# Kernel optimization log

Measured on AMD Instinct MI355X. Metric: run time of the kernel, lower is better.

Reference implementation:

```python
import jax, jax.numpy as jnp
import numpy as np

B, H, W = 8, 256, 256
NF = 64          # num_feat
E = 12           # num_expert
D = NF * 4       # token dim = 256
CD = D * E       # expanded dim = 3072


def _lrelu(x):
    return jnp.where(x >= 0, x, 0.2 * x)


def _conv(x, w, stride, pad):
    return jax.lax.conv_general_dilated(
        x, w, (stride, stride), [(pad, pad), (pad, pad)],
        dimension_numbers=('NCHW', 'OIHW', 'NCHW'))


def _bn(x, g, b):
    # training-mode BatchNorm2d: batch statistics over (N, H, W)
    m = jnp.mean(x, axis=(0, 2, 3), keepdims=True)
    v = jnp.var(x, axis=(0, 2, 3), keepdims=True)
    xn = (x - m) * jax.lax.rsqrt(v + 1e-5)
    return xn * g[None, :, None, None] + b[None, :, None, None]


def setup_inputs() -> dict:
    key = jax.random.key(0)
    ks = jax.random.split(key, 16)
    s = 0.05
    d = {}
    d['x'] = jax.random.normal(ks[0], (B, 3, H, W), jnp.float32)
    d['conv0_w'] = jax.random.normal(ks[1], (NF, 3, 3, 3)) * s
    d['conv0_b'] = jnp.zeros((NF,))
    d['conv1_w'] = jax.random.normal(ks[2], (NF, NF, 4, 4)) * s
    d['bn1_g'] = jnp.ones((NF,)); d['bn1_b'] = jnp.zeros((NF,))
    d['conv2_w'] = jax.random.normal(ks[3], (2 * NF, NF, 3, 3)) * s
    d['bn2_g'] = jnp.ones((2 * NF,)); d['bn2_b'] = jnp.zeros((2 * NF,))
    d['conv3_w'] = jax.random.normal(ks[4], (2 * NF, 2 * NF, 4, 4)) * s
    d['bn3_g'] = jnp.ones((2 * NF,)); d['bn3_b'] = jnp.zeros((2 * NF,))
    d['conv4_w'] = jax.random.normal(ks[5], (4 * NF, 2 * NF, 3, 3)) * s
    d['bn4_g'] = jnp.ones((4 * NF,)); d['bn4_b'] = jnp.zeros((4 * NF,))
    d['conv5_w'] = jax.random.normal(ks[6], (4 * NF, 4 * NF, 3, 3)) * s
    d['bn5_g'] = jnp.ones((4 * NF,)); d['bn5_b'] = jnp.zeros((4 * NF,))
    d['conv6_w'] = jax.random.normal(ks[7], (4 * NF, 4 * NF, 3, 3)) * s
    d['bn6_g'] = jnp.ones((4 * NF,)); d['bn6_b'] = jnp.zeros((4 * NF,))
    d['w_gating'] = jax.random.normal(ks[8], (D, E))          # torch.randn init
    d['body_w'] = jax.random.normal(ks[9], (D, CD)) * s       # Linear(c_dim, c_dim*blocks)
    d['body_b'] = jnp.zeros((CD,))
    d['ortho_w'] = jax.random.normal(ks[10], (1, 1, CD))      # OrthorTransform weight
    d['cls_w1'] = jax.random.normal(ks[11], (D, NF // 2)) * s # shared classifier
    d['cls_b1'] = jnp.zeros((NF // 2,))
    d['cls_w2'] = jax.random.normal(ks[12], (NF // 2, 1)) * s
    d['cls_b2'] = jnp.zeros((1,))
    return d


def reference(x, conv0_w, conv0_b, conv1_w, bn1_g, bn1_b, conv2_w, bn2_g, bn2_b,
              conv3_w, bn3_g, bn3_b, conv4_w, bn4_g, bn4_b, conv5_w, bn5_g, bn5_b,
              conv6_w, bn6_g, bn6_b, w_gating, body_w, body_b, ortho_w,
              cls_w1, cls_b1, cls_w2, cls_b2):
    # --- FE conv stack ---
    h = _lrelu(_conv(x, conv0_w, 1, 1) + conv0_b[None, :, None, None])
    h = _lrelu(_bn(_conv(h, conv1_w, 2, 1), bn1_g, bn1_b))
    h = _lrelu(_bn(_conv(h, conv2_w, 1, 1), bn2_g, bn2_b))
    h = _lrelu(_bn(_conv(h, conv3_w, 2, 1), bn3_g, bn3_b))
    h = _lrelu(_bn(_conv(h, conv4_w, 1, 1), bn4_g, bn4_b))
    h = _lrelu(_bn(_conv(h, conv5_w, 1, 1), bn5_g, bn5_b))
    h = _lrelu(_bn(_conv(h, conv6_w, 1, 1), bn6_g, bn6_b))
    b, c, hh, ww = h.shape
    tok = h.reshape(b, c, hh * ww).transpose(0, 2, 1)            # (B, N, D)
    # --- softmax router ---
    routing = jax.nn.softmax(jnp.einsum('bnd,de->bne', tok, w_gating), axis=-1)
    # --- CodeReduction: Linear + lrelu, OrthorTransform multiply, lrelu ---
    feat = _lrelu(tok @ body_w + body_b)                         # (B, N, E*D)
    feat = _lrelu(feat * ortho_w)
    feat = feat.reshape(b, hh * ww, E, D)                        # torch.split chunks
    # --- shared expert MLP on every chunk (all classifiers alias one module) ---
    hid = _lrelu(jnp.einsum('bned,df->bnef', feat, cls_w1) + cls_b1)
    outs = (jnp.einsum('bnef,fo->bneo', hid, cls_w2) + cls_b2)[..., 0]  # (B,N,E)
    # --- top-1 select (equivalent to the torch.where cascade) ---
    idx = jnp.argmax(routing, axis=-1, keepdims=True)
    output = jnp.take_along_axis(outs, idx, axis=-1)             # (B, N, 1)
    return output
```

## Files before the change

kernel.cpp:

```cpp
#include <hip/hip_runtime.h>

__device__ __forceinline__ float lrelu(float x) { return x >= 0.f ? x : 0.2f * x; }

typedef const __attribute__((address_space(1))) void* gas_ptr;
typedef __attribute__((address_space(3))) void* las_ptr;

__global__ __launch_bounds__(256) void conv0_k(const float* __restrict__ x,
                                               const float* __restrict__ w,
                                               const float* __restrict__ bias,
                                               float* __restrict__ out) {
    __shared__ float sIn[3][34][34];
    __shared__ float sW[27][16];
    const int H = 256;
    int tid = threadIdx.x, tx = tid & 31, ty = tid >> 5;
    int tX = (blockIdx.x & 7) * 32, tY = (blockIdx.x >> 3) * 32;
    int b = blockIdx.y, cog = blockIdx.z * 16;
    float acc[4][16] = {};
    const float* inB = x + (size_t)b * 3 * H * H;
    for (int idx = tid; idx < 3 * 1156; idx += 256) {
        int ci = idx / 1156, r = idx % 1156, iy = r / 34, ix = r % 34;
        int gy = tY - 1 + iy, gx = tX - 1 + ix;
        float v = 0.f;
        if ((unsigned)gy < 256u && (unsigned)gx < 256u)
            v = inB[(ci * H + gy) * H + gx];
        sIn[ci][iy][ix] = v;
    }
    for (int idx = tid; idx < 27 * 16; idx += 256) {
        int co = idx & 15, rest = idx >> 4;
        sW[rest][co] = w[(cog + co) * 27 + rest];
    }
    __syncthreads();
#pragma unroll
    for (int ci = 0; ci < 3; ci++)
#pragma unroll
        for (int dy = 0; dy < 3; dy++)
#pragma unroll
            for (int dx = 0; dx < 3; dx++) {
                float a0 = sIn[ci][ty + dy][tx + dx];
                float a1 = sIn[ci][ty + 8 + dy][tx + dx];
                float a2 = sIn[ci][ty + 16 + dy][tx + dx];
                float a3 = sIn[ci][ty + 24 + dy][tx + dx];
                const float* wp = sW[ci * 9 + dy * 3 + dx];
#pragma unroll
                for (int co = 0; co < 16; co++) {
                    float wv = wp[co];
                    acc[0][co] += a0 * wv; acc[1][co] += a1 * wv;
                    acc[2][co] += a2 * wv; acc[3][co] += a3 * wv;
                }
            }
    float* outB = out + (size_t)(b * 64 + cog) * 67080;
#pragma unroll
    for (int co = 0; co < 16; co++) {
        float bv = bias[cog + co];
#pragma unroll
        for (int r = 0; r < 4; r++)
            outB[(size_t)co * 67080 + (size_t)(tY + ty + 8 * r + 1) * 260 +
                 tX + tx + 1] = lrelu(acc[r][co] + bv);
    }
}

template <int COG, int RPT>
__device__ __forceinline__ void stats_epi(float (&acc)[RPT][COG], float2* sRed,
                                          double2* part, int cog, int slotBase,
                                          int S, int tid) {
    const int lane = tid & 63, wv = tid >> 6;
    float s[COG], q[COG];
#pragma unroll
    for (int c = 0; c < COG; c++) {
        float ss = 0.f, qq = 0.f;
#pragma unroll
        for (int j = 0; j < RPT; j++) { float v = acc[j][c]; ss += v; qq += v * v; }
        s[c] = ss; q[c] = qq;
    }
#pragma unroll
    for (int off = 32; off; off >>= 1)
#pragma unroll
        for (int c = 0; c < COG; c++) {
            s[c] += __shfl_xor(s[c], off);
            q[c] += __shfl_xor(q[c], off);
        }
    if (lane == 0)
#pragma unroll
        for (int c = 0; c < COG; c++) sRed[wv * COG + c] = make_float2(s[c], q[c]);
    __syncthreads();
    if (tid < COG) {
        double ss = 0.0, qq = 0.0;
#pragma unroll
        for (int wvi = 0; wvi < 4; wvi++) {
            float2 p = sRed[wvi * COG + tid];
            ss += (double)p.x; qq += (double)p.y;
        }
        int slot = slotBase + blockIdx.y * gridDim.x + blockIdx.x;
        part[(size_t)(cog + tid) * S + slot] = make_double2(ss, qq);
    }
}

template <int COG>
__global__ __launch_bounds__(256) void c4x4p_k(const float* __restrict__ in,
                                               const float* __restrict__ w,
                                               float* __restrict__ out,
                                               double2* __restrict__ part,
                                               int slotBase, int S,
                                               int Cin, int Cout, int Hin,
                                               int Hp, int Wp,
                                               int oHp, int oWp, int oOff) {
    __shared__ float sIn[2][4488];
    __shared__ float sW[2][16 * COG];
    __shared__ float2 sRed[4 * COG];
    const int Hout = Hin >> 1;
    const int tid = threadIdx.x, tx = tid & 31, ty = tid >> 5;
    const int tpr = Hout >> 5;
    const int tX = (blockIdx.x % tpr) * 32, tY = (blockIdx.x / tpr) * 32;
    const int b = blockIdx.y, cog = blockIdx.z * COG;
    const int HWin = Hp * Wp;
    const float* inB = in + (size_t)b * Cin * HWin;
    const int wvbase = tid & ~63;

    int gOff[5]; int lOff[5]; bool act[5];
#pragma unroll
    for (int r = 0; r < 5; r++) {
        int idx = tid + r * 256;
        bool a = idx < 1122;
        int row = idx / 17, c4 = idx % 17;
        gOff[r] = a ? ((2 * tY + row) * Wp + 2 * tX + 4 * c4) : 0;
        lOff[r] = (r * 256 + wvbase) * 4;
        act[r] = a;
    }
    const int wco = tid % COG, wt = tid / COG;
    const int wgo = ((cog + wco) * Cin) * 16 + wt;
    const bool wact = tid < 16 * COG;

    float acc[4][COG];
#pragma unroll
    for (int j = 0; j < 4; j++)
#pragma unroll
        for (int c = 0; c < COG; c++) acc[j][c] = 0.f;

#pragma unroll
    for (int r = 0; r < 5; r++)
        if (act[r])
            __builtin_amdgcn_global_load_lds((gas_ptr)(inB + gOff[r]),
                                             (las_ptr)(&sIn[0][lOff[r]]), 16, 0, 0);
    if (wact)
        __builtin_amdgcn_global_load_lds((gas_ptr)(w + wgo),
                                         (las_ptr)(&sW[0][wvbase]), 4, 0, 0);
    __syncthreads();

    for (int k = 0; k < Cin; k++) {
        const int cur = k & 1, nb = cur ^ 1;
        const bool more = (k + 1) < Cin;
        if (more) {
            const float* p = inB + (size_t)(k + 1) * HWin;
#pragma unroll
            for (int r = 0; r < 5; r++)
                if (act[r])
                    __builtin_amdgcn_global_load_lds(
                        (gas_ptr)(p + gOff[r]),
                        (las_ptr)(&sIn[nb][lOff[r]]), 16, 0, 0);
            if (wact)
                __builtin_amdgcn_global_load_lds(
                    (gas_ptr)(w + wgo + (k + 1) * 16),
                    (las_ptr)(&sW[nb][wvbase]), 4, 0, 0);
        }
        const float* sI = sIn[cur];
        const float* sw = sW[cur];
#pragma unroll
        for (int dy = 0; dy < 4; dy++)
#pragma unroll
            for (int dx = 0; dx < 4; dx++) {
                const float* bp = sI + (2 * ty + dy) * 68 + 2 * tx + dx;
                float a0 = bp[0];
                float a1 = bp[16 * 68];
                float a2 = bp[32 * 68];
                float a3 = bp[48 * 68];
                const float* wp = sw + (dy * 4 + dx) * COG;
#pragma unroll
                for (int c = 0; c < COG; c++) {
                    float wv = wp[c];
                    acc[0][c] += a0 * wv; acc[1][c] += a1 * wv;
                    acc[2][c] += a2 * wv; acc[3][c] += a3 * wv;
                }
            }
        __syncthreads();
    }

    float* outB = out + (size_t)(b * Cout + cog) * oHp * oWp;
#pragma unroll
    for (int c = 0; c < COG; c++)
#pragma unroll
        for (int r = 0; r < 4; r++)
            outB[(size_t)c * oHp * oWp +
                 (size_t)(tY + ty + 8 * r + oOff) * oWp + tX + tx + oOff] =
                acc[r][c];
    stats_epi<COG, 4>(acc, sRed, part, cog, slotBase, S, tid);
}

template <int COG>
__global__ __launch_bounds__(256) void c3x3_k(const float* __restrict__ in,
                                              const float* __restrict__ w,
                                              float* __restrict__ out,
                                              double2* __restrict__ part,
                                              int slotBase, int S,
                                              int Cin, int Cout, int H,
                                              int Hp, int Wp,
                                              int oHp, int oWp, int oOff) {
    constexpr int RS = 36;
    constexpr int ROWS = 66;
    constexpr int CI = ROWS * RS;
    constexpr int NSF4 = 2 * ROWS * 9;
    constexpr int NR = 5;
    __shared__ float sIn[2][2 * CI];
    __shared__ float sW[2][18 * COG];
    __shared__ float2 sRed[4 * COG];
    const int tid = threadIdx.x, tx = tid & 31, ty = tid >> 5;
    const int tpr = H >> 5;
    const int tX = (blockIdx.x % tpr) * 32, tY = (blockIdx.x / tpr) * 64;
    const int b = blockIdx.y, cog = blockIdx.z * COG;
    const int HWin = Hp * Wp;
    const float* inB = in + (size_t)b * Cin * HWin;
    const int wvbase = tid & ~63;

    int gOff[NR]; int lOff[NR]; bool act[NR];
#pragma unroll
    for (int r = 0; r < NR; r++) {
        int idx = tid + r * 256;
        bool a = idx < NSF4;
        int ci = idx / (9 * ROWS), rem = idx % (9 * ROWS);
        int row = rem / 9, c4 = rem % 9;
        gOff[r] = a ? (ci * HWin + (tY + row) * Wp + tX + 4 * c4) : 0;
        lOff[r] = (r * 256 + wvbase) * 4;
        act[r] = a;
    }
    const bool wact = tid < 18 * COG;
    int wgo;
    {
        int co = tid % COG, rest = tid / COG;
        int ci = rest / 9, t = rest % 9;
        wgo = ((cog + co) * Cin + ci) * 9 + t;
    }

    float acc[8][COG];
#pragma unroll
    for (int j = 0; j < 8; j++)
#pragma unroll
        for (int c = 0; c < COG; c++) acc[j][c] = 0.f;

    const int steps = Cin >> 1;

#pragma unroll
    for (int r = 0; r < NR; r++)
        if (act[r])
            __builtin_amdgcn_global_load_lds(
                (gas_ptr)(inB + gOff[r]),
                (las_ptr)(&sIn[0][lOff[r]]), 16, 0, 0);
    if (wact)
        __builtin_amdgcn_global_load_lds((gas_ptr)(w + wgo),
                                         (las_ptr)(&sW[0][wvbase]), 4, 0, 0);
    __syncthreads();

    for (int k = 0; k < steps; k++) {
        const int cur = k & 1;
        const int nb = cur ^ 1;
        const bool more = (k + 1) < steps;
        if (more) {
            const int c0n = 2 * (k + 1);
            const float* p = inB + (size_t)c0n * HWin;
#pragma unroll
            for (int r = 0; r < NR; r++)
                if (act[r])
                    __builtin_amdgcn_global_load_lds(
                        (gas_ptr)(p + gOff[r]),
                        (las_ptr)(&sIn[nb][lOff[r]]), 16, 0, 0);
            if (wact)
                __builtin_amdgcn_global_load_lds(
                    (gas_ptr)(w + (size_t)c0n * 9 + wgo),
                    (las_ptr)(&sW[nb][wvbase]), 4, 0, 0);
        }
        const float* sI = sIn[cur];
        const float* sw = sW[cur];
#pragma unroll
        for (int ci = 0; ci < 2; ci++)
#pragma unroll
            for (int dx = 0; dx < 3; dx++) {
                const float* bp = sI + ci * CI + (8 * ty) * RS + tx + dx;
                float a[10];
#pragma unroll
                for (int j = 0; j < 10; j++) a[j] = bp[j * RS];
#pragma unroll
                for (int dy = 0; dy < 3; dy++) {
                    const float* wp = sw + (ci * 9 + dy * 3 + dx) * COG;
#pragma unroll
                    for (int c = 0; c < COG; c++) {
                        float wv = wp[c];
#pragma unroll
                        for (int j = 0; j < 8; j++)
                            acc[j][c] += a[j + dy] * wv;
                    }
                }
            }
        __syncthreads();
    }

    float* outB = out + (size_t)(b * Cout + cog) * oHp * oWp;
#pragma unroll
    for (int c = 0; c < COG; c++)
#pragma unroll
        for (int j = 0; j < 8; j++)
            outB[(size_t)c * oHp * oWp +
                 (size_t)(tY + 8 * ty + j + oOff) * oWp + tX + tx + oOff] =
                acc[j][c];
    stats_epi<COG, 8>(acc, sRed, part, cog, slotBase, S, tid);
}

__global__ void bnfin_k(const double2* __restrict__ part, int S, int C, double invN,
                        const float* __restrict__ g, const float* __restrict__ bb,
                        float2* __restrict__ ss) {
    int c = threadIdx.x;
    if (c >= C) return;
    double sum = 0.0, sq = 0.0;
    for (int s = 0; s < S; s++) {
        double2 p = part[(size_t)c * S + s];
        sum += p.x; sq += p.y;
    }
    double m = sum * invN;
    double v = sq * invN - m * m;
    double sc = (double)g[c] / sqrt(v + 1e-5);
    ss[c] = make_float2((float)sc, (float)((double)bb[c] - m * sc));
}

__global__ __launch_bounds__(256) void bnact_k(float* __restrict__ p,
                                               const float2* __restrict__ ss,
                                               int C, int H, int W,
                                               int Hp, int Wp) {
    int pc = blockIdx.x;
    int c = pc & (C - 1);
    float2 t = ss ? ss[c] : make_float2(1.f, 0.f);
    bool xf = (ss != nullptr);
    float* pl = p + (size_t)pc * Hp * Wp;
    int n = Hp * Wp;
    for (int i = threadIdx.x; i < n; i += 256) {
        int y = i / Wp, x = i - y * Wp;
        bool inter = (y >= 1) && (y <= H) && (x >= 1) && (x <= W);
        if (!inter) pl[i] = 0.f;
        else if (xf) { float v = pl[i]; pl[i] = lrelu(t.x * v + t.y); }
    }
}

__global__ __launch_bounds__(256) void transp_k(const float* __restrict__ h6,
                                                const float2* __restrict__ ss,
                                                float* __restrict__ tok) {
    __shared__ float sT[32][33];
    int tx = threadIdx.x & 31, ty = threadIdx.x >> 5;
    int n0 = blockIdx.x * 32, d0 = blockIdx.y * 32, b = blockIdx.z;
    const float* hb = h6 + ((size_t)b * 256 + d0) * 4096 + n0;
#pragma unroll
    for (int r = 0; r < 4; r++) {
        int d = ty + 8 * r;
        float2 t = ss[d0 + d];
        sT[d][tx] = lrelu(t.x * hb[d * 4096 + tx] + t.y);
    }
    __syncthreads();
    float* tb = tok + ((size_t)b * 4096 + n0) * 256 + d0;
#pragma unroll
    for (int r = 0; r < 4; r++) {
        int n = ty + 8 * r;
        tb[n * 256 + tx] = sT[tx][n];
    }
}

__global__ __launch_bounds__(256) void token_k(const float* __restrict__ tok,
                                               const float* __restrict__ wg,
                                               const float* __restrict__ bw,
                                               const float* __restrict__ bb,
                                               const float* __restrict__ ow,
                                               const float* __restrict__ w1,
                                               const float* __restrict__ b1,
                                               const float* __restrict__ w2,
                                               const float* __restrict__ b2,
                                               float* __restrict__ outp) {
    __shared__ float sf[4][256];
    const int tid = threadIdx.x, wave = tid >> 6, l = tid & 63;
    const int t = blockIdx.x * 4 + wave;
    const float4 tv = reinterpret_cast<const float4*>(tok + (size_t)t * 256)[l];
    sf[wave][4 * l + 0] = tv.x; sf[wave][4 * l + 1] = tv.y;
    sf[wave][4 * l + 2] = tv.z; sf[wave][4 * l + 3] = tv.w;

    float lg[12];
#pragma unroll
    for (int e = 0; e < 12; e++) lg[e] = 0.f;
    const float tj[4] = {tv.x, tv.y, tv.z, tv.w};
#pragma unroll
    for (int j = 0; j < 4; j++) {
        const float* wr = wg + (4 * l + j) * 12;
#pragma unroll
        for (int e = 0; e < 12; e++) lg[e] += tj[j] * wr[e];
    }
#pragma unroll
    for (int off = 32; off > 0; off >>= 1) {
#pragma unroll
        for (int e = 0; e < 12; e++) lg[e] += __shfl_xor(lg[e], off);
    }
    int idx = 0; float best = lg[0];
#pragma unroll
    for (int e = 1; e < 12; e++)
        if (lg[e] > best) { best = lg[e]; idx = e; }
    const int cb = idx * 256;

    float f0 = 0.f, f1 = 0.f, f2 = 0.f, f3 = 0.f;
    const float* bwp = bw + cb + 4 * l;
#pragma unroll 4
    for (int d = 0; d < 256; d++) {
        const float td = sf[wave][d];
        const float4 wv = *reinterpret_cast<const float4*>(bwp + (size_t)d * 3072);
        f0 += td * wv.x; f1 += td * wv.y;
        f2 += td * wv.z; f3 += td * wv.w;
    }
    float fj[4] = {f0, f1, f2, f3};
#pragma unroll
    for (int j = 0; j < 4; j++) {
        int jj = cb + 4 * l + j;
        float v = lrelu(fj[j] + bb[jj]);
        v = lrelu(v * ow[jj]);
        sf[wave][4 * l + j] = v;
    }

    float o = 0.f;
    if (l < 32) {
        float h = b1[l];
#pragma unroll 4
        for (int j = 0; j < 256; j++) h += sf[wave][j] * w1[j * 32 + l];
        h = lrelu(h);
        o = h * w2[l];
    }
    o += __shfl_xor(o, 16); o += __shfl_xor(o, 8); o += __shfl_xor(o, 4);
    o += __shfl_xor(o, 2);  o += __shfl_xor(o, 1);
    if (l == 0) outp[t] = o + b2[0];
}

extern "C" void kernel_launch(void* const* d_in, const int* in_sizes, int n_in,
                              void* d_out, int out_size, void* d_ws, size_t ws_size,
                              hipStream_t stream) {
    const float* x   = (const float*)d_in[0];
    const float* w0  = (const float*)d_in[1];
    const float* b0  = (const float*)d_in[2];
    const float* w1  = (const float*)d_in[3];
    const float* g1  = (const float*)d_in[4];
    const float* be1 = (const float*)d_in[5];
    const float* w2  = (const float*)d_in[6];
    const float* g2  = (const float*)d_in[7];
    const float* be2 = (const float*)d_in[8];
    const float* w3  = (const float*)d_in[9];
    const float* g3  = (const float*)d_in[10];
    const float* be3 = (const float*)d_in[11];
    const float* w4  = (const float*)d_in[12];
    const float* g4  = (const float*)d_in[13];
    const float* be4 = (const float*)d_in[14];
    const float* w5  = (const float*)d_in[15];
    const float* g5  = (const float*)d_in[16];
    const float* be5 = (const float*)d_in[17];
    const float* w6  = (const float*)d_in[18];
    const float* g6  = (const float*)d_in[19];
    const float* be6 = (const float*)d_in[20];
    const float* wg  = (const float*)d_in[21];
    const float* bw  = (const float*)d_in[22];
    const float* bbp = (const float*)d_in[23];
    const float* owp = (const float*)d_in[24];
    const float* cw1 = (const float*)d_in[25];
    const float* cb1 = (const float*)d_in[26];
    const float* cw2 = (const float*)d_in[27];
    const float* cb2 = (const float*)d_in[28];

    char* W = (char*)d_ws;
    float2* ssb = (float2*)W;
    float2* ss1 = ssb;
    float2* ss2 = ssb + 64;
    float2* ss3 = ssb + 192;
    float2* ss4 = ssb + 320;
    float2* ss5 = ssb + 576;
    float2* ss6 = ssb + 832;
    double2* part = (double2*)(W + 16384);

    char* BIG = W + 278528;
    float* h0p = (float*)(BIG);
    float* h1p = (float*)(BIG + 70287360);
    float* h2p = (float*)(BIG);
    float* h3p = (float*)(BIG + 70287360);
    float* h4p = (float*)(BIG);
    float* h5p = (float*)(BIG + 36765696);
    float* h6  = (float*)(BIG);
    float* tok = (float*)(BIG + 36765696);

    bnact_k<<<256, 256, 0, stream>>>(h0p, nullptr, 64, 256, 256, 258, 260);
    for (int half = 0; half < 2; half++) {
        conv0_k<<<dim3(64, 4, 4), 256, 0, stream>>>(
            x + (size_t)half * 4 * 3 * 65536, w0, b0, h0p);
        c4x4p_k<8><<<dim3(16, 4, 8), 256, 0, stream>>>(
            h0p, w1, h1p + (size_t)half * 4 * 64 * 17160, part, half * 64, 128,
            64, 64, 256, 258, 260, 130, 132, 1);
    }
    bnfin_k<<<1, 256, 0, stream>>>(part, 128, 64, 1.0 / 131072.0, g1, be1, ss1);
    bnact_k<<<512, 256, 0, stream>>>(h1p, ss1, 64, 128, 128, 130, 132);
    c3x3_k<8><<<dim3(8, 8, 16), 256, 0, stream>>>(
        h1p, w2, h2p, part, 0, 64, 64, 128, 128, 130, 132, 130, 132, 1);
    bnfin_k<<<1, 256, 0, stream>>>(part, 64, 128, 1.0 / 131072.0, g2, be2, ss2);
    bnact_k<<<1024, 256, 0, stream>>>(h2p, ss2, 128, 128, 128, 130, 132);
    c4x4p_k<8><<<dim3(4, 8, 16), 256, 0, stream>>>(
        h2p, w3, h3p, part, 0, 32, 128, 128, 128, 130, 132, 66, 68, 1);
    bnfin_k<<<1, 256, 0, stream>>>(part, 32, 128, 1.0 / 32768.0, g3, be3, ss3);
    bnact_k<<<1024, 256, 0, stream>>>(h3p, ss3, 128, 64, 64, 66, 68);
    c3x3_k<8><<<dim3(2, 8, 32), 256, 0, stream>>>(
        h3p, w4, h4p, part, 0, 16, 128, 256, 64, 66, 68, 66, 68, 1);
    bnfin_k<<<1, 256, 0, stream>>>(part, 16, 256, 1.0 / 32768.0, g4, be4, ss4);
    bnact_k<<<2048, 256, 0, stream>>>(h4p, ss4, 256, 64, 64, 66, 68);
    c3x3_k<8><<<dim3(2, 8, 32), 256, 0, stream>>>(
        h4p, w5, h5p, part, 0, 16, 256, 256, 64, 66, 68, 66, 68, 1);
    bnfin_k<<<1, 256, 0, stream>>>(part, 16, 256, 1.0 / 32768.0, g5, be5, ss5);
    bnact_k<<<2048, 256, 0, stream>>>(h5p, ss5, 256, 64, 64, 66, 68);
    c3x3_k<8><<<dim3(2, 8, 32), 256, 0, stream>>>(
        h5p, w6, h6, part, 0, 16, 256, 256, 64, 66, 68, 64, 64, 0);
    bnfin_k<<<1, 256, 0, stream>>>(part, 16, 256, 1.0 / 32768.0, g6, be6, ss6);
    transp_k<<<dim3(128, 8, 8), 256, 0, stream>>>(h6, ss6, tok);
    token_k<<<8192, 256, 0, stream>>>(tok, wg, bw, bbp, owp, cw1, cb1, cw2, cb2,
                                      (float*)d_out);
}
```

Measured before the change: 2.568 ms.

## Triple-buffer c3x3 conv input staging with counted vmcnt waits

Adds a PIPE variant of the 3x3 conv kernel that keeps three LDS buffers and prefetches two channel-pair steps ahead. It replaces the full __syncthreads after each step with an s_waitcnt vmcnt(6) plus a single barrier. Idle waves issue dummy loads into a scratch LDS slot so every wave has the same number of outstanding loads and the counter stays consistent. The goal is to hide global-to-LDS load latency in the 64x64 layers, at the cost of more LDS per block (possibly lower occupancy) and fragile reliance on the load counts.

```diff
diff --git a/kernel.cpp b/kernel.cpp
--- a/kernel.cpp
+++ b/kernel.cpp
@@ -195,7 +195,7 @@
     stats_epi<COG, 4>(acc, sRed, part, cog, slotBase, S, tid);
 }
 
-template <int COG>
+template <int COG, bool PIPE>
 __global__ __launch_bounds__(256) void c3x3_k(const float* __restrict__ in,
                                               const float* __restrict__ w,
                                               float* __restrict__ out,
@@ -209,10 +209,13 @@
     constexpr int CI = ROWS * RS;
     constexpr int NSF4 = 2 * ROWS * 9;
     constexpr int NR = 5;
-    __shared__ float sIn[2][2 * CI];
-    __shared__ float sW[2][18 * COG];
+    constexpr int NBUF = PIPE ? 3 : 2;
+    __shared__ float sIn[NBUF][2 * CI];
+    __shared__ float sW[NBUF][18 * COG];
     __shared__ float2 sRed[4 * COG];
+    __shared__ alignas(16) float sDummy[64];
     const int tid = threadIdx.x, tx = tid & 31, ty = tid >> 5;
+    const bool lane0 = (tid & 63) == 0;
     const int tpr = H >> 5;
     const int tX = (blockIdx.x % tpr) * 32, tY = (blockIdx.x / tpr) * 64;
     const int b = blockIdx.y, cog = blockIdx.z * COG;
@@ -220,18 +223,19 @@
     const float* inB = in + (size_t)b * Cin * HWin;
     const int wvbase = tid & ~63;
 
-    int gOff[NR]; int lOff[NR]; bool act[NR];
+    int gOff[NR]; int lOff[NR]; bool act[NR]; bool aw[NR];
 #pragma unroll
     for (int r = 0; r < NR; r++) {
         int idx = tid + r * 256;
-        bool a = idx < NSF4;
+        act[r] = idx < NSF4;
+        aw[r] = (r * 256 + wvbase) < NSF4;
         int ci = idx / (9 * ROWS), rem = idx % (9 * ROWS);
         int row = rem / 9, c4 = rem % 9;
-        gOff[r] = a ? (ci * HWin + (tY + row) * Wp + tX + 4 * c4) : 0;
+        gOff[r] = act[r] ? (ci * HWin + (tY + row) * Wp + tX + 4 * c4) : 0;
         lOff[r] = (r * 256 + wvbase) * 4;
-        act[r] = a;
     }
     const bool wact = tid < 18 * COG;
+    const bool waw = wvbase < 18 * COG;
     int wgo;
     {
         int co = tid % COG, rest = tid / COG;
@@ -247,37 +251,42 @@
 
     const int steps = Cin >> 1;
 
-#pragma unroll
-    for (int r = 0; r < NR; r++)
-        if (act[r])
-            __builtin_amdgcn_global_load_lds(
-                (gas_ptr)(inB + gOff[r]),
-                (las_ptr)(&sIn[0][lOff[r]]), 16, 0, 0);
-    if (wact)
-        __builtin_amdgcn_global_load_lds((gas_ptr)(w + wgo),
-                                         (las_ptr)(&sW[0][wvbase]), 4, 0, 0);
-    __syncthreads();
-
-    for (int k = 0; k < steps; k++) {
-        const int cur = k & 1;
-        const int nb = cur ^ 1;
-        const bool more = (k + 1) < steps;
-        if (more) {
-            const int c0n = 2 * (k + 1);
-            const float* p = inB + (size_t)c0n * HWin;
-#pragma unroll
-            for (int r = 0; r < NR; r++)
+    auto STAGE = [&](int t, int buf) {
+        const float* p = inB + (size_t)(2 * t) * HWin;
+#pragma unroll
+        for (int r = 0; r < NR; r++) {
+            if constexpr (PIPE) {
+                float* dst = act[r] ? &sIn[buf][lOff[r]] : sDummy;
+                const float* src = act[r] ? (p + gOff[r]) : p;
+                if (act[r] || (!aw[r] && lane0))
+                    __builtin_amdgcn_global_load_lds((gas_ptr)src, (las_ptr)dst,
+                                                     16, 0, 0);
+            } else {
                 if (act[r])
                     __builtin_amdgcn_global_load_lds(
                         (gas_ptr)(p + gOff[r]),
-                        (las_ptr)(&sIn[nb][lOff[r]]), 16, 0, 0);
-            if (wact)
-                __builtin_amdgcn_global_load_lds(
-                    (gas_ptr)(w + (size_t)c0n * 9 + wgo),
-                    (las_ptr)(&sW[nb][wvbase]), 4, 0, 0);
-        }
-        const float* sI = sIn[cur];
-        const float* sw = sW[cur];
+                        (las_ptr)(&sIn[buf][lOff[r]]), 16, 0, 0);
+            }
+        }
+        {
+            const float* wsrc = w + (size_t)(2 * t) * 9 + wgo;
+            if constexpr (PIPE) {
+                const float* src = wact ? wsrc : w;
+                float* dst = wact ? &sW[buf][wvbase] : sDummy;
+                if (wact || (!waw && lane0))
+                    __builtin_amdgcn_global_load_lds((gas_ptr)src, (las_ptr)dst,
+                                                     4, 0, 0);
+            } else {
+                if (wact)
+                    __builtin_amdgcn_global_load_lds(
+                        (gas_ptr)wsrc, (las_ptr)(&sW[buf][wvbase]), 4, 0, 0);
+            }
+        }
+    };
+
+    auto COMPUTE = [&](int buf) {
+        const float* sI = sIn[buf];
+        const float* sw = sW[buf];
 #pragma unroll
         for (int ci = 0; ci < 2; ci++)
 #pragma unroll
@@ -298,7 +307,33 @@
                     }
                 }
             }
+    };
+
+    if constexpr (PIPE) {
+        STAGE(0, 0);
+        STAGE(1, 1);
+        int cur = 0, nx2 = 2;
+        for (int k = 0; k < steps; k++) {
+            if (k < steps - 1) asm volatile("s_waitcnt vmcnt(6)" ::: "memory");
+            else               asm volatile("s_waitcnt vmcnt(0)" ::: "memory");
+            __builtin_amdgcn_sched_barrier(0);
+            __builtin_amdgcn_s_barrier();
+            __builtin_amdgcn_sched_barrier(0);
+            if (k + 2 < steps) STAGE(k + 2, nx2);
+            COMPUTE(cur);
+            cur = (cur == 2) ? 0 : cur + 1;
+            nx2 = (nx2 == 2) ? 0 : nx2 + 1;
+        }
         __syncthreads();
+    } else {
+        STAGE(0, 0);
+        __syncthreads();
+        for (int k = 0; k < steps; k++) {
+            const int cur = k & 1, nb = cur ^ 1;
+            if (k + 1 < steps) STAGE(k + 1, nb);
+            COMPUTE(cur);
+            __syncthreads();
+        }
     }
 
     float* outB = out + (size_t)(b * Cout + cog) * oHp * oWp;
@@ -500,7 +535,7 @@
     }
     bnfin_k<<<1, 256, 0, stream>>>(part, 128, 64, 1.0 / 131072.0, g1, be1, ss1);
     bnact_k<<<512, 256, 0, stream>>>(h1p, ss1, 64, 128, 128, 130, 132);
-    c3x3_k<8><<<dim3(8, 8, 16), 256, 0, stream>>>(
+    c3x3_k<8, false><<<dim3(8, 8, 16), 256, 0, stream>>>(
         h1p, w2, h2p, part, 0, 64, 64, 128, 128, 130, 132, 130, 132, 1);
     bnfin_k<<<1, 256, 0, stream>>>(part, 64, 128, 1.0 / 131072.0, g2, be2, ss2);
     bnact_k<<<1024, 256, 0, stream>>>(h2p, ss2, 128, 128, 128, 130, 132);
@@ -508,15 +543,15 @@
         h2p, w3, h3p, part, 0, 32, 128, 128, 128, 130, 132, 66, 68, 1);
     bnfin_k<<<1, 256, 0, stream>>>(part, 32, 128, 1.0 / 32768.0, g3, be3, ss3);
     bnact_k<<<1024, 256, 0, stream>>>(h3p, ss3, 128, 64, 64, 66, 68);
-    c3x3_k<8><<<dim3(2, 8, 32), 256, 0, stream>>>(
+    c3x3_k<8, true><<<dim3(2, 8, 32), 256, 0, stream>>>(
         h3p, w4, h4p, part, 0, 16, 128, 256, 64, 66, 68, 66, 68, 1);
     bnfin_k<<<1, 256, 0, stream>>>(part, 16, 256, 1.0 / 32768.0, g4, be4, ss4);
     bnact_k<<<2048, 256, 0, stream>>>(h4p, ss4, 256, 64, 64, 66, 68);
-    c3x3_k<8><<<dim3(2, 8, 32), 256, 0, stream>>>(
+    c3x3_k<8, true><<<dim3(2, 8, 32), 256, 0, stream>>>(
         h4p, w5, h5p, part, 0, 16, 256, 256, 64, 66, 68, 66, 68, 1);
     bnfin_k<<<1, 256, 0, stream>>>(part, 16, 256, 1.0 / 32768.0, g5, be5, ss5);
     bnact_k<<<2048, 256, 0, stream>>>(h5p, ss5, 256, 64, 64, 66, 68);
-    c3x3_k<8><<<dim3(2, 8, 32), 256, 0, stream>>>(
+    c3x3_k<8, true><<<dim3(2, 8, 32), 256, 0, stream>>>(
         h5p, w6, h6, part, 0, 16, 256, 256, 64, 66, 68, 64, 64, 0);
     bnfin_k<<<1, 256, 0, stream>>>(part, 16, 256, 1.0 / 32768.0, g6, be6, ss6);
     transp_k<<<dim3(128, 8, 8), 256, 0, stream>>>(h6, ss6, tok);
```

Result: no change. 2.525 ms (-1.7%).
